# Kernel tuning notes

Hardware: AMD Instinct MI355X
Metric: run time of the kernel (lower is better)

The kernel has to match this reference:

```python
import jax, jax.numpy as jnp
import numpy as np

D_MODEL = 2048
N_HEADS = 16
HEAD_DIM = D_MODEL // N_HEADS
LN_EPS = 1e-6  # flax.linen.LayerNorm default
NEG_INF = float('-inf')


def _layernorm_scale_only(x, scale):
    # flax LayerNorm with use_bias=False: normalize over last axis, scale only
    mean = jnp.mean(x, axis=-1, keepdims=True)
    var = jnp.var(x, axis=-1, keepdims=True)
    return (x - mean) * jax.lax.rsqrt(var + LN_EPS) * scale


def setup_inputs() -> dict:
    key = jax.random.key(0)
    ks = jax.random.split(key, 4)
    B, S = 2, 2048
    x = jax.random.normal(ks[0], (B, S, D_MODEL), dtype=jnp.float32)
    Wqkv = jax.random.normal(ks[1], (D_MODEL, 3 * D_MODEL), dtype=jnp.float32) * 0.02
    q_ln_scale = jnp.ones((D_MODEL,), dtype=jnp.float32)
    k_ln_scale = jnp.ones((D_MODEL,), dtype=jnp.float32)
    out_W = jax.random.normal(ks[2], (D_MODEL, D_MODEL), dtype=jnp.float32) * 0.02
    return {"x": x, "Wqkv": Wqkv, "q_ln_scale": q_ln_scale,
            "k_ln_scale": k_ln_scale, "out_W": out_W}


def reference(x, Wqkv, q_ln_scale, k_ln_scale, out_W):
    B, S, _ = x.shape
    qkv = jnp.einsum('bsd,de->bse', x, Wqkv)  # [B,S,3*D] (no bias)
    q, k, v = jnp.split(qkv, 3, axis=-1)
    # QK LayerNorm (attn_qk_ln=True, no bias)
    q = _layernorm_scale_only(q, q_ln_scale)
    k = _layernorm_scale_only(k, k_ln_scale)
    # split heads: [B,S,H,Dh]
    q = q.reshape(B, S, N_HEADS, HEAD_DIM)
    k = k.reshape(B, S, N_HEADS, HEAD_DIM)
    v = v.reshape(B, S, N_HEADS, HEAD_DIM)
    # scaled scores [B,H,S,S]
    scores = jnp.einsum('bshd,bthd->bhst', q / jnp.sqrt(jnp.float32(HEAD_DIM)), k)
    # causal mask: triu(ones, k=1) marks strictly-future positions -> -inf
    causal = jnp.triu(jnp.ones((S, S), dtype=bool), 1)
    scores = jnp.where(causal, NEG_INF, scores)
    # kv-cache mask: arange(S) < S - past_position - S = 0 -> all False (no-op
    # with past_position=0 and no layer_past), faithfully omitted.
    attn = jax.nn.softmax(scores, axis=-1)
    ctx = jnp.einsum('bhst,bthd->bshd', attn, v)  # [B,S,H,Dh]
    out = jnp.einsum('bsd,de->bse', ctx.reshape(B, S, D_MODEL), out_W)
    return out
```

## Files before the change

### kernel.cpp

```cpp
#include <hip/hip_runtime.h>


typedef float f32x4 __attribute__((ext_vector_type(4)));
typedef short s16x8 __attribute__((ext_vector_type(8)));
typedef short s16x4 __attribute__((ext_vector_type(4)));

static __device__ __forceinline__ unsigned short f2bf(float f) {
  unsigned u = __builtin_bit_cast(unsigned, f);
  unsigned r = u + 0x7fffu + ((u >> 16) & 1u);
  return (unsigned short)(r >> 16);
}
static __device__ __forceinline__ float bf2f(unsigned short s) {
  unsigned u = ((unsigned)s) << 16;
  return __builtin_bit_cast(float, u);
}

static __device__ __forceinline__ void gload_lds16(const unsigned short* g, unsigned short* l) {
  __builtin_amdgcn_global_load_lds((const __attribute__((address_space(1))) void*)g,
                                   (__attribute__((address_space(3))) void*)l, 16, 0, 0);
}

__global__ __launch_bounds__(256) void k_pre(const float4* __restrict__ x,
                                             s16x4* __restrict__ xb,
                                             const float* __restrict__ Wqkv,
                                             unsigned short* __restrict__ wT,
                                             const float* __restrict__ outW,
                                             unsigned short* __restrict__ owT) {
  __shared__ float tile[32][33];
  const int bid = blockIdx.x, t = threadIdx.x;
  if (bid < 8192) {
    int i = bid * 256 + t;
    float4 v = x[i];
    s16x4 o = { (short)f2bf(v.x), (short)f2bf(v.y), (short)f2bf(v.z), (short)f2bf(v.w) };
    xb[i] = o;
    return;
  }
  const float* in;
  unsigned short* out;
  int K = 2048, N, n0, k0;
  if (bid < 20480) {
    int b2 = bid - 8192;
    in = Wqkv; out = wT; N = 6144;
    n0 = (b2 % 192) * 32; k0 = (b2 / 192) * 32;
  } else {
    int b2 = bid - 20480;
    in = outW; out = owT; N = 2048;
    n0 = (b2 & 63) * 32; k0 = (b2 >> 6) * 32;
  }
  const int tx = t & 31, ty = t >> 5;
#pragma unroll
  for (int rr = 0; rr < 4; ++rr) {
    int kr = ty + rr * 8;
    tile[kr][tx] = in[(size_t)(k0 + kr) * N + n0 + tx];
  }
  __syncthreads();
#pragma unroll
  for (int rr = 0; rr < 4; ++rr) {
    int nr = ty + rr * 8;
    out[(size_t)(n0 + nr) * K + k0 + tx] = f2bf(tile[tx][nr]);
  }
}

template <int BF16OUT, int NFN, int MINW>
__global__ __launch_bounds__(256, MINW) void k_gw(const unsigned short* __restrict__ A,
                                                  const unsigned short* __restrict__ Bt,
                                                  void* __restrict__ Cout,
                                                  int N, int K, int npx) {
  __shared__ unsigned short sA[2 * 128 * 32];
  __shared__ unsigned short sB[2 * NFN * 32 * 32];
  const int t = threadIdx.x;
  const int wid = t >> 6, lane = t & 63, g = lane >> 4, l15 = lane & 15;
  const int wm = wid >> 1, wn = wid & 1;

  const int xcd = (int)blockIdx.x & 7, idx = (int)blockIdx.x >> 3;
  const int m0 = (idx / npx) * 128;
  const int n0 = (xcd * npx + idx % npx) * (NFN * 32);

  const int u = (t & 7) ^ ((t >> 3) & 7);
  const int srow = 2 * (t >> 3) + (u >> 2);
  const int sk = (u & 3) * 8;
  const unsigned short* pA = A  + (size_t)(m0 + srow) * K + sk;
  const unsigned short* pB = Bt + (size_t)(n0 + srow) * K + sk;

  auto stage = [&](int kt, int buf) {
#pragma unroll
    for (int j = 0; j < 2; ++j)
      gload_lds16(pA + (size_t)(j * 64) * K + kt * 32,
                  sA + buf * 4096 + j * 2048 + t * 8);
#pragma unroll
    for (int j = 0; j < NFN / 2; ++j)
      gload_lds16(pB + (size_t)(j * 64) * K + kt * 32,
                  sB + buf * (NFN * 1024) + j * 2048 + t * 8);
  };

  const int si = (((l15 & 1) * 4 + g) ^ ((l15 >> 1) & 7));
  const int baseA = (wm * 32 + (l15 >> 1)) * 64 + si * 8;
  const int baseB = (wn * NFN * 8 + (l15 >> 1)) * 64 + si * 8;

  f32x4 acc[4][NFN];
#pragma unroll
  for (int fm = 0; fm < 4; ++fm)
#pragma unroll
    for (int fn = 0; fn < NFN; ++fn) acc[fm][fn] = (f32x4){0.f, 0.f, 0.f, 0.f};

  const int NK = K >> 5;
  stage(0, 0); stage(1, 1);
  if constexpr (NFN == 8) asm volatile("s_waitcnt vmcnt(6)" ::: "memory");
  else                    asm volatile("s_waitcnt vmcnt(4)" ::: "memory");
  __builtin_amdgcn_sched_barrier(0);
  __builtin_amdgcn_s_barrier();

  for (int s = 0; s < NK; ++s) {
    const unsigned short* aT = sA + (s & 1) * 4096;
    const unsigned short* bT = sB + (s & 1) * (NFN * 1024);

    s16x8 af[4];
#pragma unroll
    for (int fm = 0; fm < 4; ++fm) af[fm] = *(const s16x8*)&aT[baseA + fm * 512];
    __builtin_amdgcn_s_setprio(1);
#pragma unroll
    for (int fn = 0; fn < NFN; ++fn) {
      s16x8 bf = *(const s16x8*)&bT[baseB + fn * 512];
#pragma unroll
      for (int fm = 0; fm < 4; ++fm)
        acc[fm][fn] = __builtin_amdgcn_mfma_f32_16x16x32_bf16(af[fm], bf, acc[fm][fn], 0, 0, 0);
    }
    __builtin_amdgcn_s_setprio(0);

    __builtin_amdgcn_sched_barrier(0);
    __builtin_amdgcn_s_barrier();
    if (s + 2 < NK) {
      stage(s + 2, s & 1);
      if constexpr (NFN == 8) asm volatile("s_waitcnt vmcnt(6)" ::: "memory");
      else                    asm volatile("s_waitcnt vmcnt(4)" ::: "memory");
    } else if (s + 1 < NK) {
      asm volatile("s_waitcnt vmcnt(0)" ::: "memory");
    }
    __builtin_amdgcn_sched_barrier(0);
    __builtin_amdgcn_s_barrier();
  }

#pragma unroll
  for (int fm = 0; fm < 4; ++fm)
#pragma unroll
    for (int fn = 0; fn < NFN; ++fn)
#pragma unroll
      for (int r = 0; r < 4; ++r) {
        const int row = m0 + wm * 64 + fm * 16 + g * 4 + r;
        const int col = n0 + wn * (NFN * 16) + fn * 16 + l15;
        if (BF16OUT)
          ((unsigned short*)Cout)[(size_t)row * N + col] = f2bf(acc[fm][fn][r]);
        else
          ((float*)Cout)[(size_t)row * N + col] = acc[fm][fn][r];
      }
}

__global__ __launch_bounds__(256) void k_lnvt(unsigned short* __restrict__ qkv,
                                              const float* __restrict__ qsc,
                                              const float* __restrict__ ksc,
                                              unsigned short* __restrict__ vt) {
  __shared__ union {
    float red[8];
    unsigned short tl[64][136];
  } sm;
  const int bid = blockIdx.x, t = threadIdx.x;
  if (bid < 4096) {
    const int w = t >> 6;
    unsigned short* base = qkv + (size_t)bid * 6144;
#pragma unroll
    for (int part = 0; part < 2; ++part) {
      unsigned short* p = base + part * 2048 + t * 8;
      s16x8 v = *(const s16x8*)p;
      float f[8], s = 0.f, q = 0.f;
#pragma unroll
      for (int j = 0; j < 8; j++) { f[j] = bf2f((unsigned short)v[j]); s += f[j]; q += f[j] * f[j]; }
#pragma unroll
      for (int m = 1; m < 64; m <<= 1) { s += __shfl_xor(s, m); q += __shfl_xor(q, m); }
      __syncthreads();
      if ((t & 63) == 0) { sm.red[w] = s; sm.red[4 + w] = q; }
      __syncthreads();
      s = sm.red[0] + sm.red[1] + sm.red[2] + sm.red[3];
      q = sm.red[4] + sm.red[5] + sm.red[6] + sm.red[7];
      float mean = s * (1.f / 2048.f);
      float var = q * (1.f / 2048.f) - mean * mean;
      float inv = rsqrtf(var + 1e-6f);
      const float* sc = part ? ksc : qsc;
      float extra = part ? 1.0f : 0.12751743f;
      s16x8 o;
#pragma unroll
      for (int j = 0; j < 8; j++) o[j] = (short)f2bf((f[j] - mean) * inv * (sc[t * 8 + j] * extra));
      *(s16x8*)p = o;
    }
    return;
  }
  const int b2 = bid - 4096;
  const int bh = b2 >> 5;
  const int b = bh >> 4, h = bh & 15;
  const int s0 = (b2 & 31) * 64;
#pragma unroll
  for (int it = 0; it < 4; ++it) {
    int flat = it * 256 + t;
    int r = flat >> 4, c = flat & 15;
    s16x8 v = *(const s16x8*)(qkv + (size_t)(b * 2048 + s0 + r) * 6144 + 4096 + h * 128 + c * 8);
    *((s16x8*)&sm.tl[r][c * 8]) = v;
  }
  __syncthreads();
#pragma unroll
  for (int it = 0; it < 4; ++it) {
    int flat = it * 256 + t;
    int d = flat >> 3, cs = flat & 7;
    s16x8 o;
#pragma unroll
    for (int e = 0; e < 8; e++) {
      int key = (cs >> 2) * 32 + (e >> 2) * 16 + (cs & 3) * 4 + (e & 3);
      o[e] = (short)sm.tl[key][d];
    }
    *(s16x8*)(vt + (size_t)(bh * 128 + d) * 2048 + s0 + cs * 8) = o;
  }
}

__global__ __launch_bounds__(512, 4) void k_attn(const unsigned short* __restrict__ qkv,
                                                 const unsigned short* __restrict__ vt,
                                                 unsigned short* __restrict__ ctx) {
  __shared__ unsigned short sK[2][64 * 128];
  __shared__ unsigned short sV[2][128 * 64];
  const int t = threadIdx.x;
  const int w = t >> 6, lane = t & 63, g = lane >> 4, l15 = lane & 15;
  const int qt = 15 - (int)blockIdx.x, h = blockIdx.y, b = blockIdx.z;
  const int q0 = qt * 128;
  const int NT = 2 * qt + 2;
  const unsigned short* kbase = qkv + (size_t)(b * 2048) * 6144 + 2048 + h * 128;
  const unsigned short* vbase = vt + (size_t)((b * 16 + h) * 128) * 2048;

  auto issue_kv = [&](int k0, int bufi) {
#pragma unroll
    for (int it2 = 0; it2 < 2; ++it2) {
      int flat = it2 * 512 + t;
      int r = flat >> 4, c = flat & 15;
      gload_lds16(kbase + (size_t)(k0 + r) * 6144 + ((c ^ (r & 15)) * 8),
                  (unsigned short*)&sK[bufi][flat * 8]);
    }
#pragma unroll
    for (int it2 = 0; it2 < 2; ++it2) {
      int flat = it2 * 512 + t;
      int d = flat >> 3, z = flat & 7;
      gload_lds16(vbase + (size_t)d * 2048 + k0 + ((z ^ (d & 7)) * 8),
                  (unsigned short*)&sV[bufi][flat * 8]);
    }
  };

  s16x8 bq[4];
#pragma unroll
  for (int ks = 0; ks < 4; ++ks)
    bq[ks] = *(const s16x8*)(qkv + (size_t)(b * 2048 + q0 + w * 16 + l15) * 6144 +
                             h * 128 + (ks * 4 + g) * 8);

  f32x4 o[8];
#pragma unroll
  for (int nd = 0; nd < 8; ++nd) o[nd] = (f32x4){0.f, 0.f, 0.f, 0.f};
  float mrun = -INFINITY, lrun = 0.f;

  issue_kv(0, 0);
  int cur = 0;

  for (int kt = 0; kt < NT; ++kt) {
    if (kt + 1 < NT) {
      issue_kv((kt + 1) * 64, cur ^ 1);
      asm volatile("s_waitcnt vmcnt(4)" ::: "memory");
    } else {
      asm volatile("s_waitcnt vmcnt(0)" ::: "memory");
    }
    __builtin_amdgcn_sched_barrier(0);
    __builtin_amdgcn_s_barrier();

    const unsigned short* sKc = &sK[cur][0];
    const unsigned short* sVc = &sV[cur][0];

    f32x4 st[4];
#pragma unroll
    for (int mi = 0; mi < 4; ++mi) st[mi] = (f32x4){0.f, 0.f, 0.f, 0.f};
#pragma unroll
    for (int mi = 0; mi < 4; ++mi) {
#pragma unroll
      for (int ks = 0; ks < 4; ++ks) {
        s16x8 ak = *(const s16x8*)&sKc[(mi * 16 + l15) * 128 + (((ks * 4 + g) ^ l15) * 8)];
        st[mi] = __builtin_amdgcn_mfma_f32_16x16x32_bf16(ak, bq[ks], st[mi], 0, 0, 0);
      }
    }

    if (kt >= 2 * qt) {
      const int qglob = q0 + w * 16 + l15;
#pragma unroll
      for (int mi = 0; mi < 4; ++mi)
#pragma unroll
        for (int r = 0; r < 4; ++r)
          if (kt * 64 + mi * 16 + 4 * g + r > qglob) st[mi][r] = -INFINITY;
    }

    float mt = -INFINITY;
#pragma unroll
    for (int mi = 0; mi < 4; ++mi)
#pragma unroll
      for (int r = 0; r < 4; ++r) mt = fmaxf(mt, st[mi][r]);
    mt = fmaxf(mt, __shfl_xor(mt, 16));
    mt = fmaxf(mt, __shfl_xor(mt, 32));

    if (!__all(mt <= mrun + 8.f)) {
      const float mnew = fmaxf(mrun, mt);
      const float alpha = exp2f(mrun - mnew);
      lrun *= alpha;
      float ar[4];
#pragma unroll
      for (int r = 0; r < 4; ++r) ar[r] = __shfl(alpha, 4 * g + r);
#pragma unroll
      for (int nd = 0; nd < 8; ++nd)
#pragma unroll
        for (int r = 0; r < 4; ++r) o[nd][r] *= ar[r];
      mrun = mnew;
    }

    float ls = 0.f;
#pragma unroll
    for (int mi = 0; mi < 4; ++mi)
#pragma unroll
      for (int r = 0; r < 4; ++r) {
        float pp = exp2f(st[mi][r] - mrun);
        st[mi][r] = pp;
        ls += pp;
      }
    ls += __shfl_xor(ls, 16);
    ls += __shfl_xor(ls, 32);
    lrun += ls;

    s16x8 pa01, pa23;
#pragma unroll
    for (int j = 0; j < 8; ++j) {
      pa01[j] = (short)f2bf(st[j >> 2][j & 3]);
      pa23[j] = (short)f2bf(st[2 + (j >> 2)][j & 3]);
    }

#pragma unroll
    for (int nd = 0; nd < 8; ++nd) {
      const int d = nd * 16 + l15;
      const int zs = d & 7;
      s16x8 bv0 = *(const s16x8*)&sVc[d * 64 + ((g ^ zs) * 8)];
      s16x8 bv1 = *(const s16x8*)&sVc[d * 64 + (((4 + g) ^ zs) * 8)];
      o[nd] = __builtin_amdgcn_mfma_f32_16x16x32_bf16(pa01, bv0, o[nd], 0, 0, 0);
      o[nd] = __builtin_amdgcn_mfma_f32_16x16x32_bf16(pa23, bv1, o[nd], 0, 0, 0);
    }

    __builtin_amdgcn_sched_barrier(0);
    __builtin_amdgcn_s_barrier();
    cur ^= 1;
  }

  float ivr[4];
#pragma unroll
  for (int r = 0; r < 4; ++r) ivr[r] = 1.0f / __shfl(lrun, 4 * g + r);
#pragma unroll
  for (int nd = 0; nd < 8; ++nd) {
    const int col = h * 128 + nd * 16 + l15;
#pragma unroll
    for (int r = 0; r < 4; ++r) {
      const int row = b * 2048 + q0 + w * 16 + 4 * g + r;
      ctx[(size_t)row * 2048 + col] = f2bf(o[nd][r] * ivr[r]);
    }
  }
}

extern "C" void kernel_launch(void* const* d_in, const int* in_sizes, int n_in,
                              void* d_out, int out_size, void* d_ws, size_t ws_size,
                              hipStream_t stream) {
  (void)in_sizes; (void)n_in; (void)out_size; (void)ws_size;
  const float* x    = (const float*)d_in[0];
  const float* Wqkv = (const float*)d_in[1];
  const float* qsc  = (const float*)d_in[2];
  const float* ksc  = (const float*)d_in[3];
  const float* outW = (const float*)d_in[4];

  char* ws = (char*)d_ws;
  unsigned short* xb  = (unsigned short*)(ws);
  unsigned short* wT  = (unsigned short*)(ws + 16777216);
  unsigned short* owT = (unsigned short*)(ws + 41943040);
  unsigned short* qkv = (unsigned short*)(ws + 50331648);
  unsigned short* vt  = (unsigned short*)(ws + 100663296);
  unsigned short* ctx = xb;

  k_pre<<<24576, 256, 0, stream>>>((const float4*)x, (s16x4*)xb, Wqkv, wT, outW, owT);
  k_gw<1, 8, 3><<<768, 256, 0, stream>>>(xb, wT, qkv, 6144, 2048, 3);
  k_lnvt<<<5120, 256, 0, stream>>>(qkv, qsc, ksc, vt);
  k_attn<<<dim3(16, 16, 2), 512, 0, stream>>>(qkv, vt, ctx);
  k_gw<0, 4, 2><<<512, 256, 0, stream>>>(ctx, owT, d_out, 2048, 2048, 2);
}
```

Before: 287.2 us.

## Pair causal query tiles per attention block and add dedicated output GEMM kernel

Each attention block now processes two query tiles (qt and 15-qt) back to back, so every block does the same 34 KV iterations instead of a triangular spread of work. The block count halves to 512. The KV prefetch carries across the segment boundary, and the first tile's output is written mid-loop. The output projection moves to a new k_go kernel: a 128x128 tile with a 64-deep K step, two-stage LDS double buffering, swizzled loads, XCD-aware tile mapping and setprio around the MFMAs. This trades fewer blocks, and so less latency hiding, for balanced causal load and a tuned final GEMM.

```diff
diff --git a/kernel.cpp b/kernel.cpp
--- a/kernel.cpp
+++ b/kernel.cpp
@@ -155,6 +155,99 @@
       }
 }
 
+__global__ __launch_bounds__(256, 2) void k_go(const unsigned short* __restrict__ A,
+                                               const unsigned short* __restrict__ Bt,
+                                               float* __restrict__ Cout,
+                                               int N, int K, int npx) {
+  __shared__ unsigned short sA[2 * 128 * 64];
+  __shared__ unsigned short sB[2 * 128 * 64];
+  const int t = threadIdx.x;
+  const int wid = t >> 6, lane = t & 63, g = lane >> 4, l15 = lane & 15;
+  const int wm = wid >> 1, wn = wid & 1;
+
+  const int xcd = (int)blockIdx.x & 7, idx = (int)blockIdx.x >> 3;
+  const int m0 = (idx / npx) * 128;
+  const int n0 = (xcd * npx + idx % npx) * 128;
+
+  const int u = (t & 7) ^ ((t >> 3) & 7);
+  const unsigned short* pA = A  + (size_t)(m0 + (t >> 3)) * K + u * 8;
+  const unsigned short* pB = Bt + (size_t)(n0 + (t >> 3)) * K + u * 8;
+
+  auto stage = [&](int kt, int buf) {
+#pragma unroll
+    for (int j = 0; j < 4; ++j)
+      gload_lds16(pA + (size_t)(j * 32) * K + kt * 64,
+                  sA + buf * 8192 + j * 2048 + t * 8);
+#pragma unroll
+    for (int j = 0; j < 4; ++j)
+      gload_lds16(pB + (size_t)(j * 32) * K + kt * 64,
+                  sB + buf * 8192 + j * 2048 + t * 8);
+  };
+
+  const int x7 = l15 & 7;
+  const int sl0 = (g ^ x7) * 8, sl1 = ((4 + g) ^ x7) * 8;
+  const int baseA = (wm * 64 + l15) * 64;
+  const int baseB = (wn * 64 + l15) * 64;
+
+  f32x4 acc[4][4];
+#pragma unroll
+  for (int fm = 0; fm < 4; ++fm)
+#pragma unroll
+    for (int fn = 0; fn < 4; ++fn) acc[fm][fn] = (f32x4){0.f, 0.f, 0.f, 0.f};
+
+  const int NK = K >> 6;
+  stage(0, 0); stage(1, 1);
+  asm volatile("s_waitcnt vmcnt(8)" ::: "memory");
+  __builtin_amdgcn_sched_barrier(0);
+  __builtin_amdgcn_s_barrier();
+
+  for (int s = 0; s < NK; ++s) {
+    const unsigned short* aT = sA + (s & 1) * 8192;
+    const unsigned short* bT = sB + (s & 1) * 8192;
+
+    s16x8 af[4][2];
+#pragma unroll
+    for (int fm = 0; fm < 4; ++fm) {
+      af[fm][0] = *(const s16x8*)&aT[baseA + fm * 1024 + sl0];
+      af[fm][1] = *(const s16x8*)&aT[baseA + fm * 1024 + sl1];
+    }
+    __builtin_amdgcn_s_setprio(1);
+#pragma unroll
+    for (int fn = 0; fn < 4; ++fn) {
+      s16x8 bf0 = *(const s16x8*)&bT[baseB + fn * 1024 + sl0];
+      s16x8 bf1 = *(const s16x8*)&bT[baseB + fn * 1024 + sl1];
+#pragma unroll
+      for (int fm = 0; fm < 4; ++fm) {
+        acc[fm][fn] = __builtin_amdgcn_mfma_f32_16x16x32_bf16(af[fm][0], bf0, acc[fm][fn], 0, 0, 0);
+        acc[fm][fn] = __builtin_amdgcn_mfma_f32_16x16x32_bf16(af[fm][1], bf1, acc[fm][fn], 0, 0, 0);
+      }
+    }
+    __builtin_amdgcn_s_setprio(0);
+
+    __builtin_amdgcn_sched_barrier(0);
+    __builtin_amdgcn_s_barrier();
+    if (s + 2 < NK) {
+      stage(s + 2, s & 1);
+      asm volatile("s_waitcnt vmcnt(8)" ::: "memory");
+    } else if (s + 1 < NK) {
+      asm volatile("s_waitcnt vmcnt(0)" ::: "memory");
+    }
+    __builtin_amdgcn_sched_barrier(0);
+    __builtin_amdgcn_s_barrier();
+  }
+
+#pragma unroll
+  for (int fm = 0; fm < 4; ++fm)
+#pragma unroll
+    for (int fn = 0; fn < 4; ++fn)
+#pragma unroll
+      for (int r = 0; r < 4; ++r) {
+        const int row = m0 + wm * 64 + fm * 16 + g * 4 + r;
+        const int col = n0 + wn * 64 + fn * 16 + l15;
+        Cout[(size_t)row * N + col] = acc[fm][fn][r];
+      }
+}
+
 __global__ __launch_bounds__(256) void k_lnvt(unsigned short* __restrict__ qkv,
                                               const float* __restrict__ qsc,
                                               const float* __restrict__ ksc,
@@ -219,16 +312,17 @@
   }
 }
 
-__global__ __launch_bounds__(512, 4) void k_attn(const unsigned short* __restrict__ qkv,
-                                                 const unsigned short* __restrict__ vt,
-                                                 unsigned short* __restrict__ ctx) {
+__global__ __launch_bounds__(512) void k_attn(const unsigned short* __restrict__ qkv,
+                                              const unsigned short* __restrict__ vt,
+                                              unsigned short* __restrict__ ctx) {
   __shared__ unsigned short sK[2][64 * 128];
   __shared__ unsigned short sV[2][128 * 64];
   const int t = threadIdx.x;
   const int w = t >> 6, lane = t & 63, g = lane >> 4, l15 = lane & 15;
-  const int qt = 15 - (int)blockIdx.x, h = blockIdx.y, b = blockIdx.z;
-  const int q0 = qt * 128;
-  const int NT = 2 * qt + 2;
+  const int pair = blockIdx.x, h = blockIdx.y, b = blockIdx.z;
+  const int qt0 = 15 - pair, qt1 = pair;
+  const int n0 = 2 * qt0 + 2;
+  const int NT = 34;
   const unsigned short* kbase = qkv + (size_t)(b * 2048) * 6144 + 2048 + h * 128;
   const unsigned short* vbase = vt + (size_t)((b * 16 + h) * 128) * 2048;
 
@@ -250,28 +344,60 @@
   };
 
   s16x8 bq[4];
-#pragma unroll
-  for (int ks = 0; ks < 4; ++ks)
-    bq[ks] = *(const s16x8*)(qkv + (size_t)(b * 2048 + q0 + w * 16 + l15) * 6144 +
-                             h * 128 + (ks * 4 + g) * 8);
+  auto load_q = [&](int q0) {
+#pragma unroll
+    for (int ks = 0; ks < 4; ++ks)
+      bq[ks] = *(const s16x8*)(qkv + (size_t)(b * 2048 + q0 + w * 16 + l15) * 6144 +
+                               h * 128 + (ks * 4 + g) * 8);
+  };
 
   f32x4 o[8];
-#pragma unroll
-  for (int nd = 0; nd < 8; ++nd) o[nd] = (f32x4){0.f, 0.f, 0.f, 0.f};
-  float mrun = -INFINITY, lrun = 0.f;
-
+  float mrun, lrun;
+  auto reset_state = [&]() {
+#pragma unroll
+    for (int nd = 0; nd < 8; ++nd) o[nd] = (f32x4){0.f, 0.f, 0.f, 0.f};
+    mrun = -INFINITY; lrun = 0.f;
+  };
+  auto write_o = [&](int q0) {
+    float ivr[4];
+#pragma unroll
+    for (int r = 0; r < 4; ++r) ivr[r] = 1.0f / __shfl(lrun, 4 * g + r);
+#pragma unroll
+    for (int nd = 0; nd < 8; ++nd) {
+      const int col = h * 128 + nd * 16 + l15;
+#pragma unroll
+      for (int r = 0; r < 4; ++r) {
+        const int row = b * 2048 + q0 + w * 16 + 4 * g + r;
+        ctx[(size_t)row * 2048 + col] = f2bf(o[nd][r] * ivr[r]);
+      }
+    }
+  };
+
+  reset_state();
+  load_q(qt0 * 128);
   issue_kv(0, 0);
   int cur = 0;
 
-  for (int kt = 0; kt < NT; ++kt) {
-    if (kt + 1 < NT) {
-      issue_kv((kt + 1) * 64, cur ^ 1);
+  for (int it = 0; it < NT; ++it) {
+    const int seg = (it < n0) ? 0 : 1;
+    const int qt = seg ? qt1 : qt0;
+    const int kt = seg ? it - n0 : it;
+
+    if (it + 1 < NT) {
+      const int kn = (it + 1 < n0) ? it + 1 : it + 1 - n0;
+      issue_kv(kn * 64, cur ^ 1);
       asm volatile("s_waitcnt vmcnt(4)" ::: "memory");
     } else {
       asm volatile("s_waitcnt vmcnt(0)" ::: "memory");
     }
     __builtin_amdgcn_sched_barrier(0);
     __builtin_amdgcn_s_barrier();
+
+    if (seg == 1 && kt == 0) {
+      write_o(qt0 * 128);
+      reset_state();
+      load_q(qt1 * 128);
+    }
 
     const unsigned short* sKc = &sK[cur][0];
     const unsigned short* sVc = &sV[cur][0];
@@ -289,7 +415,7 @@
     }
 
     if (kt >= 2 * qt) {
-      const int qglob = q0 + w * 16 + l15;
+      const int qglob = qt * 128 + w * 16 + l15;
 #pragma unroll
       for (int mi = 0; mi < 4; ++mi)
 #pragma unroll
@@ -353,19 +479,7 @@
     __builtin_amdgcn_s_barrier();
     cur ^= 1;
   }
-
-  float ivr[4];
-#pragma unroll
-  for (int r = 0; r < 4; ++r) ivr[r] = 1.0f / __shfl(lrun, 4 * g + r);
-#pragma unroll
-  for (int nd = 0; nd < 8; ++nd) {
-    const int col = h * 128 + nd * 16 + l15;
-#pragma unroll
-    for (int r = 0; r < 4; ++r) {
-      const int row = b * 2048 + q0 + w * 16 + 4 * g + r;
-      ctx[(size_t)row * 2048 + col] = f2bf(o[nd][r] * ivr[r]);
-    }
-  }
+  write_o(qt1 * 128);
 }
 
 extern "C" void kernel_launch(void* const* d_in, const int* in_sizes, int n_in,
@@ -389,6 +503,6 @@
   k_pre<<<24576, 256, 0, stream>>>((const float4*)x, (s16x4*)xb, Wqkv, wT, outW, owT);
   k_gw<1, 8, 3><<<768, 256, 0, stream>>>(xb, wT, qkv, 6144, 2048, 3);
   k_lnvt<<<5120, 256, 0, stream>>>(qkv, qsc, ksc, vt);
-  k_attn<<<dim3(16, 16, 2), 512, 0, stream>>>(qkv, vt, ctx);
-  k_gw<0, 4, 2><<<512, 256, 0, stream>>>(ctx, owT, d_out, 2048, 2048, 2);
-}
+  k_attn<<<dim3(8, 16, 2), 512, 0, stream>>>(qkv, vt, ctx);
+  k_go<<<512, 256, 0, stream>>>(ctx, owT, (float*)d_out, 2048, 2048, 2);
+}
```

Result: faster. 262.7 us (-8.6%).
